# Kernel optimization log

Hardware: AMD Instinct MI355X
Metric: run time of the kernel (lower is better)

## Reference

```python
import jax, jax.numpy as jnp
import numpy as np

N = 160000   # total nodes
G = 800      # total graphs (B * 50)
NPG = 200    # nodes per graph
E = 1280000  # total edges (avg degree 8)
B = 16       # proteins
K = 2        # TAGConv hops
IN_F = 31
HID = 64


def setup_inputs() -> dict:
    key = jax.random.key(0)
    ks = jax.random.split(key, 16)
    s = 0.1
    x = jax.random.normal(ks[0], (N, IN_F), jnp.float32)
    src = jax.random.randint(ks[1], (E,), 0, N, jnp.int32)
    dst = jax.random.randint(ks[2], (E,), 0, N, jnp.int32)
    node2graph = jnp.repeat(jnp.arange(G, dtype=jnp.int32), NPG)
    W0 = jax.random.normal(ks[3], (IN_F * (K + 1), HID), jnp.float32) * s
    b0 = jax.random.normal(ks[4], (HID,), jnp.float32) * s
    W1 = jax.random.normal(ks[5], (HID * (K + 1), HID), jnp.float32) * s
    b1 = jax.random.normal(ks[6], (HID,), jnp.float32) * s
    W2 = jax.random.normal(ks[7], (HID * (K + 1), HID), jnp.float32) * s
    b2 = jax.random.normal(ks[8], (HID,), jnp.float32) * s
    W3 = jax.random.normal(ks[9], (HID * (K + 1), HID), jnp.float32) * s
    b3 = jax.random.normal(ks[10], (HID,), jnp.float32) * s
    Wg = jax.random.normal(ks[11], (HID, 1), jnp.float32) * s
    bg = jax.random.normal(ks[12], (1,), jnp.float32) * s
    return dict(x=x, src=src, dst=dst, node2graph=node2graph,
                W0=W0, b0=b0, W1=W1, b1=b1, W2=W2, b2=b2, W3=W3, b3=b3,
                Wg=Wg, bg=bg)


def reference(x, src, dst, node2graph, W0, b0, W1, b1, W2, b2, W3, b3, Wg, bg):
    # symmetric normalization: norm = in_degree^{-1/2}, clamped at 1 (DGL TAGConv)
    deg = jax.ops.segment_sum(jnp.ones((E,), x.dtype), dst, num_segments=N)
    norm = jax.lax.rsqrt(jnp.clip(deg, 1.0))[:, None]  # [N,1]

    def tag_conv(h, W, b):
        hops = [h]
        for _ in range(K):
            h = norm * jax.ops.segment_sum((h * norm)[src], dst, num_segments=N)
            hops.append(h)
        return jnp.concatenate(hops, axis=-1) @ W + b

    h = x
    for W, b in ((W0, b0), (W1, b1), (W2, b2), (W3, b3)):
        h = jax.nn.relu(tag_conv(h, W, b))

    # GlobalAttentionPooling: per-graph softmax over gate logits, weighted sum
    gate = h @ Wg + bg  # [N,1]
    gmax = jax.ops.segment_max(gate, node2graph, num_segments=G)  # [G,1]
    e = jnp.exp(gate - gmax[node2graph])
    z = jax.ops.segment_sum(e, node2graph, num_segments=G)
    alpha = e / z[node2graph]
    readout = jax.ops.segment_sum(alpha * h, node2graph, num_segments=G)  # [G,64]
    return readout.reshape(B, 50, HID)
```

## Files before the change

### kernel.cpp

```cpp
#include <hip/hip_runtime.h>

#define NN 160000
#define NE 1280000
#define NG 800
#define NPGR 200
#define INF_ 31
#define HID 64

#define NBUK 256
#define NPBK 625
#define BCAP 6144
#define CHUNK 8192

typedef unsigned short bfu;
typedef __attribute__((ext_vector_type(8))) short short8;
typedef __attribute__((ext_vector_type(4))) float f32x4;

__device__ inline float bflo(unsigned u) { return __uint_as_float(u << 16); }
__device__ inline float bfhi(unsigned u) { return __uint_as_float(u & 0xffff0000u); }
__device__ inline float bfs(bfu s) { return __uint_as_float(((unsigned)s) << 16); }
__device__ inline unsigned f2bf(float x) {
  unsigned u = __float_as_uint(x);
  return (u + 0x7fffu + ((u >> 16) & 1u)) >> 16;
}
__device__ inline unsigned pack2(float a, float b) {
  return f2bf(a) | (f2bf(b) << 16);
}
__device__ inline void unpack8(uint4 v, float* f) {
  f[0] = bflo(v.x); f[1] = bfhi(v.x);
  f[2] = bflo(v.y); f[3] = bfhi(v.y);
  f[4] = bflo(v.z); f[5] = bfhi(v.z);
  f[6] = bflo(v.w); f[7] = bfhi(v.w);
}

__global__ __launch_bounds__(256) void k_izero(int* __restrict__ p, int n) {
  int i = blockIdx.x * 256 + threadIdx.x;
  if (i < n) p[i] = 0;
}

__global__ __launch_bounds__(256) void k_deg(const int* __restrict__ dst,
                                             int* __restrict__ deg, int E) {
  int e = blockIdx.x * 256 + threadIdx.x;
  if (e < E) atomicAdd(&deg[dst[e]], 1);
}

__global__ __launch_bounds__(256) void k_border(const int* __restrict__ deg,
                                                int* __restrict__ order) {
  __shared__ int hist[64], cur[64];
  int b = blockIdx.x, tid = threadIdx.x;
  int nbase = b * NPBK;
  if (tid < 64) hist[tid] = 0;
  __syncthreads();
  for (int i = tid; i < NPBK; i += 256)
    atomicAdd(&hist[min(deg[nbase + i], 63)], 1);
  __syncthreads();
  if (tid == 0) {
    int s = 0;
    for (int k = 0; k < 64; ++k) { cur[k] = s; s += hist[k]; }
  }
  __syncthreads();
  for (int i = tid; i < NPBK; i += 256) {
    int nid = nbase + i;
    int pos = atomicAdd(&cur[min(deg[nid], 63)], 1);
    order[nbase + pos] = nid;
  }
}

__global__ __launch_bounds__(256) void k_pad(const float* __restrict__ x,
                                             bfu* __restrict__ xb) {
  int i = blockIdx.x * 256 + threadIdx.x;
  int n = i >> 5, f = i & 31;
  float v = (f < INF_) ? x[(size_t)n * INF_ + f] : 0.f;
  xb[i] = (bfu)f2bf(v);
}

__global__ __launch_bounds__(256) void k_wfrag(const float* __restrict__ W,
                                               short* __restrict__ Wf) {
  int idx = blockIdx.x * 256 + threadIdx.x;
  int lane = idx & 63, t = (idx >> 6) & 3, step = idx >> 8;
  int col = t * 16 + (lane & 15);
  int kbase = step * 32 + ((lane >> 4) & 3) * 8;
  short8 o;
#pragma unroll
  for (int j = 0; j < 8; ++j)
    o[j] = (short)f2bf(W[(size_t)(kbase + j) * 64 + col]);
  *reinterpret_cast<short8*>(&Wf[(size_t)idx * 8]) = o;
}

__global__ __launch_bounds__(256) void k_wfrag0(const float* __restrict__ W0,
                                                short* __restrict__ Wf) {
  int idx = blockIdx.x * 256 + threadIdx.x;
  int lane = idx & 63, t = (idx >> 6) & 3, step = idx >> 8;
  int col = t * 16 + (lane & 15);
  int kbase = step * 32 + ((lane >> 4) & 3) * 8;
  short8 o;
#pragma unroll
  for (int j = 0; j < 8; ++j) {
    int r = kbase + j, pp = r >> 5, ir = r & 31;
    float v = (ir < INF_) ? W0[(size_t)(pp * INF_ + ir) * 64 + col] : 0.f;
    o[j] = (short)f2bf(v);
  }
  *reinterpret_cast<short8*>(&Wf[(size_t)idx * 8]) = o;
}

__global__ __launch_bounds__(256) void k_scan1(const int* __restrict__ in,
    int* __restrict__ out, int* __restrict__ bsum, int n) {
  __shared__ int sh[256];
  int tid = threadIdx.x;
  int base = blockIdx.x * 1024 + tid * 4;
  int v0 = (base + 0 < n) ? in[base + 0] : 0;
  int v1 = (base + 1 < n) ? in[base + 1] : 0;
  int v2 = (base + 2 < n) ? in[base + 2] : 0;
  int v3 = (base + 3 < n) ? in[base + 3] : 0;
  int t0 = v0, t1 = t0 + v1, t2 = t1 + v2, t3 = t2 + v3;
  sh[tid] = t3;
  __syncthreads();
  for (int off = 1; off < 256; off <<= 1) {
    int x = (tid >= off) ? sh[tid - off] : 0;
    __syncthreads();
    sh[tid] += x;
    __syncthreads();
  }
  int excl = (tid > 0) ? sh[tid - 1] : 0;
  if (base + 0 < n) out[base + 0] = excl;
  if (base + 1 < n) out[base + 1] = excl + t0;
  if (base + 2 < n) out[base + 2] = excl + t1;
  if (base + 3 < n) out[base + 3] = excl + t2;
  if (bsum && tid == 255) bsum[blockIdx.x] = sh[255];
}

__global__ __launch_bounds__(256) void k_scanadd(const int* __restrict__ part,
    const int* __restrict__ boff, int* __restrict__ rp, int n, int Etot) {
  int i = blockIdx.x * 256 + threadIdx.x;
  if (i < n) {
    rp[i] = part[i] + boff[i >> 10];
    if (i == 0) rp[n] = Etot;
  }
}

__global__ __launch_bounds__(256) void k_gcinit(int* __restrict__ gcur) {
  gcur[threadIdx.x] = threadIdx.x * BCAP;
}

__global__ __launch_bounds__(256) void k_bucket(const int* __restrict__ src,
    const int* __restrict__ dst, int* __restrict__ gcur,
    uint2* __restrict__ buk, int E) {
  __shared__ uint2 stage[CHUNK];
  __shared__ int cnt[NBUK], gbase[NBUK];
  int tid = threadIdx.x;
  int base = blockIdx.x * CHUNK;
  int nch = min(CHUNK, E - base);
  for (int i = tid; i < NBUK; i += 256) cnt[i] = 0;
  __syncthreads();
  for (int i = tid; i < nch; i += 256) {
    int s = src[base + i], d = dst[base + i];
    stage[i] = make_uint2((unsigned)s, (unsigned)d);
    atomicAdd(&cnt[(unsigned)d / NPBK], 1);
  }
  __syncthreads();
  for (int i = tid; i < NBUK; i += 256) {
    gbase[i] = atomicAdd(&gcur[i], cnt[i]);
    cnt[i] = 0;
  }
  __syncthreads();
  for (int i = tid; i < nch; i += 256) {
    uint2 r = stage[i];
    int b = r.y / NPBK;
    int off = atomicAdd(&cnt[b], 1);
    buk[(size_t)gbase[b] + off] = r;
  }
}

__global__ __launch_bounds__(256) void k_scat2(const uint2* __restrict__ buk,
    const int* __restrict__ gcur, const int* __restrict__ rp,
    const int* __restrict__ deg, unsigned* __restrict__ csr) {
  __shared__ int cur[NPBK];
  int b = blockIdx.x, tid = threadIdx.x;
  int nbase = b * NPBK;
  for (int i = tid; i < NPBK; i += 256) cur[i] = rp[nbase + i];
  __syncthreads();
  int cnt = gcur[b] - b * BCAP;
  const uint2* __restrict__ bp = buk + (size_t)b * BCAP;
  for (int i = tid; i < cnt; i += 256) {
    uint2 r = bp[i];
    int pos = atomicAdd(&cur[r.y - nbase], 1);
    unsigned d = min((unsigned)deg[r.x], 16383u);
    csr[pos] = (d << 18) | r.x;
  }
}

template<int F>
__global__ __launch_bounds__(256) void k_gather(const bfu* __restrict__ hin,
    const int* __restrict__ rp, const unsigned* __restrict__ csr,
    const int* __restrict__ order, bfu* __restrict__ hout) {
  constexpr int LPN = F / 8;
  constexpr int NPB = 256 / LPN;
  int slot = threadIdx.x / LPN;
  int f8 = (threadIdx.x % LPN) * 8;
  int nid = order[blockIdx.x * NPB + slot];
  int beg = rp[nid], end = rp[nid + 1];
  float acc[8] = {0.f, 0.f, 0.f, 0.f, 0.f, 0.f, 0.f, 0.f};
  int e = beg;
  for (; e + 8 <= end; e += 8) {
    unsigned ed[8];
    uint4 v[8];
#pragma unroll
    for (int k = 0; k < 8; ++k) ed[k] = csr[e + k];
#pragma unroll
    for (int k = 0; k < 8; ++k)
      v[k] = *reinterpret_cast<const uint4*>(&hin[(size_t)(ed[k] & 0x3FFFFu) * F + f8]);
#pragma unroll
    for (int k = 0; k < 8; ++k) {
      float f[8];
      unpack8(v[k], f);
      float w = rsqrtf(fmaxf((float)(ed[k] >> 18), 1.0f));
#pragma unroll
      for (int q = 0; q < 8; ++q) acc[q] = fmaf(f[q], w, acc[q]);
    }
  }
  for (; e + 2 <= end; e += 2) {
    unsigned e0 = csr[e], e1 = csr[e + 1];
    uint4 v0 = *reinterpret_cast<const uint4*>(&hin[(size_t)(e0 & 0x3FFFFu) * F + f8]);
    uint4 v1 = *reinterpret_cast<const uint4*>(&hin[(size_t)(e1 & 0x3FFFFu) * F + f8]);
    float f0[8], f1[8];
    unpack8(v0, f0); unpack8(v1, f1);
    float w0 = rsqrtf(fmaxf((float)(e0 >> 18), 1.0f));
    float w1 = rsqrtf(fmaxf((float)(e1 >> 18), 1.0f));
#pragma unroll
    for (int q = 0; q < 8; ++q) {
      acc[q] = fmaf(f0[q], w0, acc[q]);
      acc[q] = fmaf(f1[q], w1, acc[q]);
    }
  }
  if (e < end) {
    unsigned e0 = csr[e];
    uint4 v0 = *reinterpret_cast<const uint4*>(&hin[(size_t)(e0 & 0x3FFFFu) * F + f8]);
    float f0[8];
    unpack8(v0, f0);
    float w0 = rsqrtf(fmaxf((float)(e0 >> 18), 1.0f));
#pragma unroll
    for (int q = 0; q < 8; ++q) acc[q] = fmaf(f0[q], w0, acc[q]);
  }
  float wn = rsqrtf(fmaxf((float)(end - beg), 1.0f));
#pragma unroll
  for (int q = 0; q < 8; ++q) acc[q] *= wn;
  uint4 o;
  o.x = pack2(acc[0], acc[1]);
  o.y = pack2(acc[2], acc[3]);
  o.z = pack2(acc[4], acc[5]);
  o.w = pack2(acc[6], acc[7]);
  *reinterpret_cast<uint4*>(&hout[(size_t)nid * F + f8]) = o;
}

template<int F>
__global__ __launch_bounds__(256) void k_gemm_mfma(const bfu* __restrict__ h0,
    const bfu* __restrict__ h1, const bfu* __restrict__ h2,
    const short* __restrict__ Wf, const float* __restrict__ bias,
    bfu* __restrict__ outb) {
  constexpr int SPP = F / 32;
  int wave = threadIdx.x >> 6, lane = threadIdx.x & 63;
  int quad = lane >> 4, l15 = lane & 15;
  int nb = blockIdx.x * 64 + wave * 16;

  f32x4 acc[4] = {{0.f,0.f,0.f,0.f}, {0.f,0.f,0.f,0.f},
                  {0.f,0.f,0.f,0.f}, {0.f,0.f,0.f,0.f}};
  const bfu* parts[3] = {h0, h1, h2};
#pragma unroll
  for (int p = 0; p < 3; ++p) {
    const bfu* __restrict__ P = parts[p] + (size_t)(nb + l15) * F + quad * 8;
#pragma unroll
    for (int s = 0; s < SPP; ++s) {
      short8 a = *reinterpret_cast<const short8*>(P + s * 32);
      int step = p * SPP + s;
      const short* __restrict__ wb = Wf + ((size_t)step * 4 * 64 + lane) * 8;
#pragma unroll
      for (int t = 0; t < 4; ++t) {
        short8 b = *reinterpret_cast<const short8*>(wb + (size_t)t * 64 * 8);
        acc[t] = __builtin_amdgcn_mfma_f32_16x16x32_bf16(a, b, acc[t], 0, 0, 0);
      }
    }
  }
#pragma unroll
  for (int t = 0; t < 4; ++t) {
    int col = t * 16 + l15;
    float bj = bias[col];
#pragma unroll
    for (int r = 0; r < 4; ++r) {
      int node = nb + quad * 4 + r;
      float v = fmaxf(acc[t][r] + bj, 0.f);
      outb[(size_t)node * 64 + col] = (bfu)f2bf(v);
    }
  }
}

__global__ __launch_bounds__(256) void k_pool(const bfu* __restrict__ h,
    const float* __restrict__ Wg, const float* __restrict__ bg,
    float* __restrict__ out) {
  int g = blockIdx.x;
  int tid = threadIdx.x;
  int lane = tid & 63, w = tid >> 6;
  const bfu* hg = h + (size_t)g * NPGR * HID;
  float wgt = Wg[lane];
  __shared__ float sgate[NPGR];
  __shared__ float sred[256];
  __shared__ float spart[4][64];

  for (int n = w; n < NPGR; n += 4) {
    float v = bfs(hg[(size_t)n * HID + lane]) * wgt;
    for (int off = 32; off > 0; off >>= 1) v += __shfl_down(v, off, 64);
    if (lane == 0) sgate[n] = v + bg[0];
  }
  __syncthreads();

  float m = -INFINITY;
  for (int n = tid; n < NPGR; n += 256) m = fmaxf(m, sgate[n]);
  sred[tid] = m;
  __syncthreads();
  for (int s = 128; s > 0; s >>= 1) {
    if (tid < s) sred[tid] = fmaxf(sred[tid], sred[tid + s]);
    __syncthreads();
  }
  float gmax = sred[0];
  __syncthreads();

  float zp = 0.f;
  for (int n = tid; n < NPGR; n += 256) {
    float e = expf(sgate[n] - gmax);
    sgate[n] = e;
    zp += e;
  }
  sred[tid] = zp;
  __syncthreads();
  for (int s = 128; s > 0; s >>= 1) {
    if (tid < s) sred[tid] += sred[tid + s];
    __syncthreads();
  }
  float z = sred[0];
  __syncthreads();

  float acc = 0.f;
  for (int n = w; n < NPGR; n += 4)
    acc += sgate[n] * bfs(hg[(size_t)n * HID + lane]);
  spart[w][lane] = acc;
  __syncthreads();
  if (w == 0) {
    float t = spart[0][lane] + spart[1][lane] + spart[2][lane] + spart[3][lane];
    out[(size_t)g * HID + lane] = t / z;
  }
}

extern "C" void kernel_launch(void* const* d_in, const int* in_sizes, int n_in,
                              void* d_out, int out_size, void* d_ws, size_t ws_size,
                              hipStream_t stream) {
  const float* x   = (const float*)d_in[0];
  const int*   src = (const int*)d_in[1];
  const int*   dst = (const int*)d_in[2];
  const float* W0 = (const float*)d_in[4];
  const float* b0 = (const float*)d_in[5];
  const float* W1 = (const float*)d_in[6];
  const float* b1 = (const float*)d_in[7];
  const float* W2 = (const float*)d_in[8];
  const float* b2 = (const float*)d_in[9];
  const float* W3 = (const float*)d_in[10];
  const float* b3 = (const float*)d_in[11];
  const float* Wg = (const float*)d_in[12];
  const float* bg = (const float*)d_in[13];
  float* out = (float*)d_out;

  const int N = NN, E = NE;
  const int NB1 = (N + 1023) / 1024;

  char* p = (char*)d_ws;
  unsigned* csr = (unsigned*)p;      p += sizeof(unsigned) * (size_t)E;
  int* deg     = (int*)p;            p += sizeof(int) * (size_t)N;
  int* part    = (int*)p;            p += sizeof(int) * (size_t)N;
  int* rp      = (int*)p;            p += sizeof(int) * (size_t)(N + 4);
  int* order   = (int*)p;            p += sizeof(int) * (size_t)N;
  int* bsum    = (int*)p;            p += sizeof(int) * 256;
  int* boff    = (int*)p;            p += sizeof(int) * 256;
  int* gcur    = (int*)p;            p += sizeof(int) * NBUK;
  short* Wf0   = (short*)p;          p += sizeof(short) * 768 * 8;
  short* Wf1   = (short*)p;          p += sizeof(short) * 1536 * 8;
  short* Wf2   = (short*)p;          p += sizeof(short) * 1536 * 8;
  short* Wf3   = (short*)p;          p += sizeof(short) * 1536 * 8;
  bfu* xb      = (bfu*)p;            p += sizeof(bfu) * (size_t)N * 32;
  bfu* h1b     = (bfu*)p;            p += sizeof(bfu) * (size_t)N * HID;
  bfu* h2b     = (bfu*)p;            p += sizeof(bfu) * (size_t)N * HID;
  bfu* hAb     = (bfu*)p;            p += sizeof(bfu) * (size_t)N * HID;
  bfu* hBb     = (bfu*)p;            p += sizeof(bfu) * (size_t)N * HID;
  uint2* buk   = (uint2*)hBb;

  k_izero<<<(N + 255) / 256, 256, 0, stream>>>(deg, N);
  k_deg<<<(E + 255) / 256, 256, 0, stream>>>(dst, deg, E);
  k_scan1<<<NB1, 256, 0, stream>>>(deg, part, bsum, N);
  k_scan1<<<1, 256, 0, stream>>>(bsum, boff, nullptr, NB1);
  k_scanadd<<<(N + 255) / 256, 256, 0, stream>>>(part, boff, rp, N, E);
  k_gcinit<<<1, NBUK, 0, stream>>>(gcur);
  k_bucket<<<(E + CHUNK - 1) / CHUNK, 256, 0, stream>>>(src, dst, gcur, buk, E);
  k_scat2<<<NBUK, 256, 0, stream>>>(buk, gcur, rp, deg, csr);
  k_border<<<NBUK, 256, 0, stream>>>(deg, order);

  k_pad<<<(N * 32) / 256, 256, 0, stream>>>(x, xb);
  k_wfrag0<<<3, 256, 0, stream>>>(W0, Wf0);
  k_wfrag<<<6, 256, 0, stream>>>(W1, Wf1);
  k_wfrag<<<6, 256, 0, stream>>>(W2, Wf2);
  k_wfrag<<<6, 256, 0, stream>>>(W3, Wf3);

  k_gather<32><<<N / 64, 256, 0, stream>>>(xb, rp, csr, order, h1b);
  k_gather<32><<<N / 64, 256, 0, stream>>>(h1b, rp, csr, order, h2b);
  k_gemm_mfma<32><<<N / 64, 256, 0, stream>>>(xb, h1b, h2b, Wf0, b0, hAb);

  const short* Wfs[3] = {Wf1, Wf2, Wf3};
  const float* bs[3] = {b1, b2, b3};
  bfu* hin = hAb;
  bfu* hout = hBb;
  for (int l = 0; l < 3; ++l) {
    k_gather<64><<<N / 32, 256, 0, stream>>>(hin, rp, csr, order, h1b);
    k_gather<64><<<N / 32, 256, 0, stream>>>(h1b, rp, csr, order, h2b);
    k_gemm_mfma<64><<<N / 64, 256, 0, stream>>>(hin, h1b, h2b, Wfs[l], bs[l], hout);
    bfu* t = hin; hin = hout; hout = t;
  }

  k_pool<<<NG, 256, 0, stream>>>(hin, Wg, bg, out);
}
```

Baseline: 671.7 us.

## Derive degrees and CSR row pointers from buckets, dropping global atomics and scans

```diff
diff --git a/kernel.cpp b/kernel.cpp
--- a/kernel.cpp
+++ b/kernel.cpp
@@ -31,39 +31,6 @@
   f[2] = bflo(v.y); f[3] = bfhi(v.y);
   f[4] = bflo(v.z); f[5] = bfhi(v.z);
   f[6] = bflo(v.w); f[7] = bfhi(v.w);
-}
-
-__global__ __launch_bounds__(256) void k_izero(int* __restrict__ p, int n) {
-  int i = blockIdx.x * 256 + threadIdx.x;
-  if (i < n) p[i] = 0;
-}
-
-__global__ __launch_bounds__(256) void k_deg(const int* __restrict__ dst,
-                                             int* __restrict__ deg, int E) {
-  int e = blockIdx.x * 256 + threadIdx.x;
-  if (e < E) atomicAdd(&deg[dst[e]], 1);
-}
-
-__global__ __launch_bounds__(256) void k_border(const int* __restrict__ deg,
-                                                int* __restrict__ order) {
-  __shared__ int hist[64], cur[64];
-  int b = blockIdx.x, tid = threadIdx.x;
-  int nbase = b * NPBK;
-  if (tid < 64) hist[tid] = 0;
-  __syncthreads();
-  for (int i = tid; i < NPBK; i += 256)
-    atomicAdd(&hist[min(deg[nbase + i], 63)], 1);
-  __syncthreads();
-  if (tid == 0) {
-    int s = 0;
-    for (int k = 0; k < 64; ++k) { cur[k] = s; s += hist[k]; }
-  }
-  __syncthreads();
-  for (int i = tid; i < NPBK; i += 256) {
-    int nid = nbase + i;
-    int pos = atomicAdd(&cur[min(deg[nid], 63)], 1);
-    order[nbase + pos] = nid;
-  }
 }
 
 __global__ __launch_bounds__(256) void k_pad(const float* __restrict__ x,
@@ -101,41 +68,6 @@
     o[j] = (short)f2bf(v);
   }
   *reinterpret_cast<short8*>(&Wf[(size_t)idx * 8]) = o;
-}
-
-__global__ __launch_bounds__(256) void k_scan1(const int* __restrict__ in,
-    int* __restrict__ out, int* __restrict__ bsum, int n) {
-  __shared__ int sh[256];
-  int tid = threadIdx.x;
-  int base = blockIdx.x * 1024 + tid * 4;
-  int v0 = (base + 0 < n) ? in[base + 0] : 0;
-  int v1 = (base + 1 < n) ? in[base + 1] : 0;
-  int v2 = (base + 2 < n) ? in[base + 2] : 0;
-  int v3 = (base + 3 < n) ? in[base + 3] : 0;
-  int t0 = v0, t1 = t0 + v1, t2 = t1 + v2, t3 = t2 + v3;
-  sh[tid] = t3;
-  __syncthreads();
-  for (int off = 1; off < 256; off <<= 1) {
-    int x = (tid >= off) ? sh[tid - off] : 0;
-    __syncthreads();
-    sh[tid] += x;
-    __syncthreads();
-  }
-  int excl = (tid > 0) ? sh[tid - 1] : 0;
-  if (base + 0 < n) out[base + 0] = excl;
-  if (base + 1 < n) out[base + 1] = excl + t0;
-  if (base + 2 < n) out[base + 2] = excl + t1;
-  if (base + 3 < n) out[base + 3] = excl + t2;
-  if (bsum && tid == 255) bsum[blockIdx.x] = sh[255];
-}
-
-__global__ __launch_bounds__(256) void k_scanadd(const int* __restrict__ part,
-    const int* __restrict__ boff, int* __restrict__ rp, int n, int Etot) {
-  int i = blockIdx.x * 256 + threadIdx.x;
-  if (i < n) {
-    rp[i] = part[i] + boff[i >> 10];
-    if (i == 0) rp[n] = Etot;
-  }
 }
 
 __global__ __launch_bounds__(256) void k_gcinit(int* __restrict__ gcur) {
@@ -171,17 +103,72 @@
   }
 }
 
+__global__ __launch_bounds__(256) void k_count(const uint2* __restrict__ buk,
+    const int* __restrict__ gcur, int* __restrict__ deg,
+    int* __restrict__ order) {
+  __shared__ int cnt[NPBK];
+  __shared__ int h64[64], c64[64];
+  int b = blockIdx.x, tid = threadIdx.x;
+  int nbase = b * NPBK;
+  for (int i = tid; i < NPBK; i += 256) cnt[i] = 0;
+  if (tid < 64) h64[tid] = 0;
+  __syncthreads();
+  int n = gcur[b] - b * BCAP;
+  const uint2* __restrict__ bp = buk + (size_t)b * BCAP;
+  for (int i = tid; i < n; i += 256) atomicAdd(&cnt[bp[i].y - nbase], 1);
+  __syncthreads();
+  for (int i = tid; i < NPBK; i += 256) {
+    int c = cnt[i];
+    deg[nbase + i] = c;
+    atomicAdd(&h64[min(c, 63)], 1);
+  }
+  __syncthreads();
+  if (tid == 0) {
+    int s = 0;
+    for (int k = 0; k < 64; ++k) { c64[k] = s; s += h64[k]; }
+  }
+  __syncthreads();
+  for (int i = tid; i < NPBK; i += 256) {
+    int pos = atomicAdd(&c64[min(cnt[i], 63)], 1);
+    order[nbase + pos] = nbase + i;
+  }
+}
+
+__global__ __launch_bounds__(256) void k_bscan(const int* __restrict__ gcur,
+                                               int* __restrict__ bktoff) {
+  __shared__ int sh[256];
+  int tid = threadIdx.x;
+  sh[tid] = gcur[tid] - tid * BCAP;
+  __syncthreads();
+  for (int off = 1; off < 256; off <<= 1) {
+    int v = (tid >= off) ? sh[tid - off] : 0;
+    __syncthreads();
+    sh[tid] += v;
+    __syncthreads();
+  }
+  bktoff[tid] = (tid > 0) ? sh[tid - 1] : 0;
+}
+
 __global__ __launch_bounds__(256) void k_scat2(const uint2* __restrict__ buk,
-    const int* __restrict__ gcur, const int* __restrict__ rp,
-    const int* __restrict__ deg, unsigned* __restrict__ csr) {
+    const int* __restrict__ gcur, const int* __restrict__ bktoff,
+    const int* __restrict__ deg, int* __restrict__ rp,
+    unsigned* __restrict__ csr) {
   __shared__ int cur[NPBK];
   int b = blockIdx.x, tid = threadIdx.x;
   int nbase = b * NPBK;
-  for (int i = tid; i < NPBK; i += 256) cur[i] = rp[nbase + i];
-  __syncthreads();
-  int cnt = gcur[b] - b * BCAP;
+  if (tid == 0) {
+    int s = bktoff[b];
+    for (int i = 0; i < NPBK; ++i) {
+      cur[i] = s;
+      rp[nbase + i] = s;
+      s += deg[nbase + i];
+    }
+    if (b == NBUK - 1) rp[NN] = NE;
+  }
+  __syncthreads();
+  int n = gcur[b] - b * BCAP;
   const uint2* __restrict__ bp = buk + (size_t)b * BCAP;
-  for (int i = tid; i < cnt; i += 256) {
+  for (int i = tid; i < n; i += 256) {
     uint2 r = bp[i];
     int pos = atomicAdd(&cur[r.y - nbase], 1);
     unsigned d = min((unsigned)deg[r.x], 16383u);
@@ -368,17 +355,14 @@
   float* out = (float*)d_out;
 
   const int N = NN, E = NE;
-  const int NB1 = (N + 1023) / 1024;
 
   char* p = (char*)d_ws;
   unsigned* csr = (unsigned*)p;      p += sizeof(unsigned) * (size_t)E;
   int* deg     = (int*)p;            p += sizeof(int) * (size_t)N;
-  int* part    = (int*)p;            p += sizeof(int) * (size_t)N;
   int* rp      = (int*)p;            p += sizeof(int) * (size_t)(N + 4);
   int* order   = (int*)p;            p += sizeof(int) * (size_t)N;
-  int* bsum    = (int*)p;            p += sizeof(int) * 256;
-  int* boff    = (int*)p;            p += sizeof(int) * 256;
   int* gcur    = (int*)p;            p += sizeof(int) * NBUK;
+  int* bktoff  = (int*)p;            p += sizeof(int) * NBUK;
   short* Wf0   = (short*)p;          p += sizeof(short) * 768 * 8;
   short* Wf1   = (short*)p;          p += sizeof(short) * 1536 * 8;
   short* Wf2   = (short*)p;          p += sizeof(short) * 1536 * 8;
@@ -390,15 +374,11 @@
   bfu* hBb     = (bfu*)p;            p += sizeof(bfu) * (size_t)N * HID;
   uint2* buk   = (uint2*)hBb;
 
-  k_izero<<<(N + 255) / 256, 256, 0, stream>>>(deg, N);
-  k_deg<<<(E + 255) / 256, 256, 0, stream>>>(dst, deg, E);
-  k_scan1<<<NB1, 256, 0, stream>>>(deg, part, bsum, N);
-  k_scan1<<<1, 256, 0, stream>>>(bsum, boff, nullptr, NB1);
-  k_scanadd<<<(N + 255) / 256, 256, 0, stream>>>(part, boff, rp, N, E);
   k_gcinit<<<1, NBUK, 0, stream>>>(gcur);
   k_bucket<<<(E + CHUNK - 1) / CHUNK, 256, 0, stream>>>(src, dst, gcur, buk, E);
-  k_scat2<<<NBUK, 256, 0, stream>>>(buk, gcur, rp, deg, csr);
-  k_border<<<NBUK, 256, 0, stream>>>(deg, order);
+  k_count<<<NBUK, 256, 0, stream>>>(buk, gcur, deg, order);
+  k_bscan<<<1, NBUK, 0, stream>>>(gcur, bktoff);
+  k_scat2<<<NBUK, 256, 0, stream>>>(buk, gcur, bktoff, deg, rp, csr);
 
   k_pad<<<(N * 32) / 256, 256, 0, stream>>>(x, xb);
   k_wfrag0<<<3, 256, 0, stream>>>(W0, Wf0);
```

New measurement: 639.2 us. -4.8%, faster.
